# Optimization experiments

Measured on AMD Instinct MI355X. Metric: run time of the kernel, lower is better.

## Reference

```python
import jax, jax.numpy as jnp
import numpy as np
import math

D_MODEL = 128
N_HEADS = 8
HEAD_DIM = D_MODEL // N_HEADS


def setup_inputs() -> dict:
    key = jax.random.key(0)
    ks = jax.random.split(key, 16)
    B, N, D = 8, 1024, D_MODEL
    s = 1.0 / math.sqrt(D)
    inp = {
        "x": jax.random.normal(ks[0], (B, N, D), dtype=jnp.float32),
        "adj_mask": jax.random.randint(ks[1], (B, N, N), 0, 2, dtype=jnp.int32),
        "edge_weights": jax.random.uniform(ks[2], (B, N, N), dtype=jnp.float32),
        "Wq": jax.random.normal(ks[3], (D, D), dtype=jnp.float32) * s,
        "bq": jnp.zeros((D,), jnp.float32),
        "Wk": jax.random.normal(ks[4], (D, D), dtype=jnp.float32) * s,
        "bk": jnp.zeros((D,), jnp.float32),
        "Wv": jax.random.normal(ks[5], (D, D), dtype=jnp.float32) * s,
        "bv": jnp.zeros((D,), jnp.float32),
        "Wo": jax.random.normal(ks[6], (D, D), dtype=jnp.float32) * s,
        "bo": jnp.zeros((D,), jnp.float32),
        "We": jax.random.normal(ks[7], (N_HEADS,), dtype=jnp.float32),  # edge_proj weight (n_heads,1) squeezed
        "be": jnp.zeros((N_HEADS,), jnp.float32),                       # edge_proj bias
    }
    return inp


def reference(x, adj_mask, edge_weights, Wq, bq, Wk, bk, Wv, bv, Wo, bo, We, be):
    B, N, D = x.shape
    H, hd = N_HEADS, HEAD_DIM
    scale = math.sqrt(hd)
    # projections -> (B, H, N, hd)
    Q = (x @ Wq + bq).reshape(B, N, H, hd).transpose(0, 2, 1, 3)
    K = (x @ Wk + bk).reshape(B, N, H, hd).transpose(0, 2, 1, 3)
    V = (x @ Wv + bv).reshape(B, N, H, hd).transpose(0, 2, 1, 3)
    # scores (B, H, N, N)
    scores = jnp.einsum('bhnd,bhmd->bhnm', Q, K) / scale
    # edge bias: Linear(1, H) applied per edge, permuted to (B, H, N, N)
    edge_bias = edge_weights[:, None, :, :] * We[None, :, None, None] + be[None, :, None, None]
    scores = scores + edge_bias
    # adjacency masking
    scores = jnp.where(adj_mask[:, None, :, :] == 0, -jnp.inf, scores)
    attn = jax.nn.softmax(scores, axis=-1)  # dropout=0 (eval)
    out = jnp.einsum('bhnm,bhmd->bhnd', attn, V)
    out = out.transpose(0, 2, 1, 3).reshape(B, N, D)
    return out @ Wo + bo
```

## Files before the change

kernel.cpp:

```cpp
#include <hip/hip_runtime.h>
#include <hip/hip_bf16.h>

typedef __attribute__((ext_vector_type(4))) short bf16x4;
typedef __attribute__((ext_vector_type(4))) float f32x4;
typedef __attribute__((ext_vector_type(4))) int i32x4;

#define LOG2E 1.4426950408889634f
#define SMAX 8.0f

static __device__ inline f32x4 mfma16(bf16x4 a, bf16x4 b, f32x4 c) {
  return __builtin_amdgcn_mfma_f32_16x16x16bf16_1k(a, b, c, 0, 0, 0);
}
static __device__ inline ushort f2bfu(float f) {
  __hip_bfloat16 h = __float2bfloat16(f);
  return *(ushort*)&h;
}
static __device__ __forceinline__ void dma16(const void* g, void* l) {
  __builtin_amdgcn_global_load_lds(
      (const __attribute__((address_space(1))) void*)g,
      (__attribute__((address_space(3))) void*)l, 16, 0, 0);
}

__global__ __launch_bounds__(256) void gemm_qkv(
    const float* __restrict__ x,
    const float* __restrict__ Wq, const float* __restrict__ bq,
    const float* __restrict__ Wk, const float* __restrict__ bk,
    const float* __restrict__ Wv, const float* __restrict__ bv,
    ushort* __restrict__ Qs, ushort* __restrict__ Kt, ushort* __restrict__ Vt) {
  const int which = blockIdx.x >> 10;
  const int bid = blockIdx.x & 1023;
  const int tid = threadIdx.x;
  const int l = tid & 63, w = tid >> 6;
  const int lm = l & 15, g = l >> 4;
  const int tile = bid * 4 + w;
  const int mt = tile >> 3, nt = tile & 7;
  const int row = mt * 16 + lm;
  const int col = nt * 16 + lm;

  const float* W = (which == 0) ? Wq : (which == 1) ? Wk : Wv;
  const float* bias = (which == 0) ? bq : (which == 1) ? bk : bv;

  f32x4 acc = {0.f, 0.f, 0.f, 0.f};
#pragma unroll
  for (int ks = 0; ks < 8; ++ks) {
    f32x4 av = *(const f32x4*)(x + (size_t)row * 128 + ks * 16 + g * 4);
    bf16x4 a;
    a[0] = (short)f2bfu(av[0]); a[1] = (short)f2bfu(av[1]);
    a[2] = (short)f2bfu(av[2]); a[3] = (short)f2bfu(av[3]);
    const float* wp = W + (size_t)(ks * 16 + g * 4) * 128 + col;
    bf16x4 b;
    b[0] = (short)f2bfu(wp[0]);   b[1] = (short)f2bfu(wp[128]);
    b[2] = (short)f2bfu(wp[256]); b[3] = (short)f2bfu(wp[384]);
    acc = mfma16(a, b, acc);
  }
  const float bv_ = bias[col];
  const float alpha = (which == 0) ? 0.25f * LOG2E : 1.0f;
  float v0 = (acc[0] + bv_) * alpha, v1 = (acc[1] + bv_) * alpha;
  float v2 = (acc[2] + bv_) * alpha, v3 = (acc[3] + bv_) * alpha;
  const int mb = mt * 16;

  if (which == 0) {
    Qs[(size_t)(mb + g * 4 + 0) * 128 + col] = f2bfu(v0);
    Qs[(size_t)(mb + g * 4 + 1) * 128 + col] = f2bfu(v1);
    Qs[(size_t)(mb + g * 4 + 2) * 128 + col] = f2bfu(v2);
    Qs[(size_t)(mb + g * 4 + 3) * 128 + col] = f2bfu(v3);
  } else if (which == 1) {
    const size_t kb = ((size_t)((mb >> 10) * 8 + nt) * 1024 + ((mb & 1023) + g * 4));
    Kt[(kb + 0) * 16 + lm] = f2bfu(v0);
    Kt[(kb + 1) * 16 + lm] = f2bfu(v1);
    Kt[(kb + 2) * 16 + lm] = f2bfu(v2);
    Kt[(kb + 3) * 16 + lm] = f2bfu(v3);
  } else {
    const size_t addr = ((size_t)((mb >> 10) * 8 + nt) * 16 + ((mb & 1023) >> 6)) * 1024
                        + (size_t)lm * 64 + (mb & 63) + g * 4;
    bf16x4 vv;
    vv[0] = (short)f2bfu(v0); vv[1] = (short)f2bfu(v1);
    vv[2] = (short)f2bfu(v2); vv[3] = (short)f2bfu(v3);
    *(bf16x4*)(Vt + addr) = vv;
  }
}

#define BUFB 40960

__global__ __launch_bounds__(512) void attn_kernel(
    const ushort* __restrict__ Qs, const ushort* __restrict__ Kt,
    const ushort* __restrict__ Vt, const int* __restrict__ adj,
    const float* __restrict__ edge, const float* __restrict__ We,
    const float* __restrict__ Wo, const float* __restrict__ bo,
    float* __restrict__ out) {
  __shared__ __align__(16) char smem[2 * BUFB];

  const int tid = threadIdx.x;
  const int l = tid & 63, h = tid >> 6;
  const int lm = l & 15, g = l >> 4;
  const int b = blockIdx.x >> 6;
  const int m0 = (blockIdx.x & 63) * 16;

  const float Weh = We[h] * LOG2E;
  const bf16x4 qf = *(const bf16x4*)(Qs + ((size_t)b * 1024 + m0 + lm) * 128 + h * 16 + g * 4);

  const ushort* kt0 = Kt + ((size_t)b * 8 + h) * 16384 + l * 8;
  const int dv = l >> 3, mv = l & 7;
  const int voff = dv * 64 + (((mv * 2) ^ (dv & 6)) * 4);
  const ushort* vt0 = Vt + ((size_t)b * 8 + h) * 16384 + voff;
  const int hh = h & 3;
  const int sr = hh * 4 + (l >> 4);
  const int sci = ((l & 15) * 4) ^ ((sr & 7) << 3);
  const int* ssrc = ((h < 4) ? adj : (const int*)edge)
                    + (size_t)b * 1048576 + (size_t)(m0 + sr) * 1024 + sci;

  char* kdst = smem + h * 2048;
  char* vdst = smem + 16384 + h * 2048;
  char* sdst = smem + ((h < 4) ? 32768 : 36864) + hh * 1024;

  float lsum = 0.f;
  f32x4 oacc = {0.f, 0.f, 0.f, 0.f};
  const f32x4 cinit = {-SMAX, -SMAX, -SMAX, -SMAX};

  auto stage = [&](int T) {
    const int bo_ = (T & 1) * BUFB;
    const ushort* ks = kt0 + (size_t)T * 1024;
    const ushort* vs = vt0 + (size_t)T * 1024;
    dma16(ks,        kdst + bo_);
    dma16(ks + 512,  kdst + bo_ + 1024);
    dma16(vs,        vdst + bo_);
    dma16(vs + 512,  vdst + bo_ + 1024);
    dma16(ssrc + T * 64, sdst + bo_);
  };

  auto compute = [&](int bi) {
    const char* base = smem + bi * BUFB;
    const char* kls = base + h * 2048;
    const char* vls = base + 16384 + h * 2048;
    const int* als = (const int*)(base + 32768);
    const int* els = (const int*)(base + 36864);
    const int xorv = (lm & 7) << 3;

    f32x4 st[4];
    bf16x4 vfr[4];
#pragma unroll
    for (int t = 0; t < 4; ++t) {
      bf16x4 kf = *(const bf16x4*)(kls + (t * 16 + lm) * 32 + g * 8);
      st[t] = mfma16(kf, qf, cinit);
      vfr[t] = *(const bf16x4*)(vls + lm * 128 + (((t * 4 + g) ^ (lm & 6)) * 8));
    }
#pragma unroll
    for (int t = 0; t < 4; ++t) {
      const int ci = (t * 16 + g * 4) ^ xorv;
      const i32x4 a4 = *(const i32x4*)(als + lm * 64 + ci);
      const i32x4 e4i = *(const i32x4*)(els + lm * 64 + ci);
      const f32x4 e4 = *(const f32x4*)&e4i;
      bf16x4 pf4;
#pragma unroll
      for (int j = 0; j < 4; ++j) {
        float p = __builtin_amdgcn_exp2f(fmaf(e4[j], Weh, st[t][j]));
        p = (a4[j] == 0) ? 0.f : p;
        lsum += p;
        pf4[j] = (short)f2bfu(p);
      }
      oacc = mfma16(vfr[t], pf4, oacc);
    }
  };

  stage(0);
  stage(1);

  for (int ct = 0; ct < 15; ++ct) {
    asm volatile("s_waitcnt vmcnt(5)" ::: "memory");
    __builtin_amdgcn_s_barrier();
    __builtin_amdgcn_sched_barrier(0);
    compute(ct & 1);
    __builtin_amdgcn_s_barrier();
    __builtin_amdgcn_sched_barrier(0);
    if (ct < 14) stage(ct + 2);
  }
  asm volatile("s_waitcnt vmcnt(0)" ::: "memory");
  __builtin_amdgcn_s_barrier();
  __builtin_amdgcn_sched_barrier(0);
  compute(1);

  lsum += __shfl_xor(lsum, 16, 64);
  lsum += __shfl_xor(lsum, 32, 64);
  const float inv = 1.0f / lsum;

  __syncthreads();
  ushort* aot = (ushort*)smem;
  {
    bf16x4 ov;
    ov[0] = (short)f2bfu(oacc[0] * inv);
    ov[1] = (short)f2bfu(oacc[1] * inv);
    ov[2] = (short)f2bfu(oacc[2] * inv);
    ov[3] = (short)f2bfu(oacc[3] * inv);
    *(bf16x4*)(aot + lm * 132 + h * 16 + g * 4) = ov;
  }
  __syncthreads();

  f32x4 acc = {0.f, 0.f, 0.f, 0.f};
#pragma unroll
  for (int ks = 0; ks < 8; ++ks) {
    bf16x4 a = *(const bf16x4*)(aot + lm * 132 + ks * 16 + g * 4);
    const float* wp = Wo + (size_t)(ks * 16 + g * 4) * 128 + h * 16 + lm;
    bf16x4 bfr;
    bfr[0] = (short)f2bfu(wp[0]);   bfr[1] = (short)f2bfu(wp[128]);
    bfr[2] = (short)f2bfu(wp[256]); bfr[3] = (short)f2bfu(wp[384]);
    acc = mfma16(a, bfr, acc);
  }
  const float bv = bo[h * 16 + lm];
  float* op = out + ((size_t)b * 1024 + m0 + g * 4) * 128 + h * 16 + lm;
  op[0 * 128] = acc[0] + bv;
  op[1 * 128] = acc[1] + bv;
  op[2 * 128] = acc[2] + bv;
  op[3 * 128] = acc[3] + bv;
}

extern "C" void kernel_launch(void* const* d_in, const int* in_sizes, int n_in,
                              void* d_out, int out_size, void* d_ws, size_t ws_size,
                              hipStream_t stream) {
  const float* x   = (const float*)d_in[0];
  const int*   adj = (const int*)d_in[1];
  const float* ew  = (const float*)d_in[2];
  const float* Wq  = (const float*)d_in[3];
  const float* bq  = (const float*)d_in[4];
  const float* Wk  = (const float*)d_in[5];
  const float* bk  = (const float*)d_in[6];
  const float* Wv  = (const float*)d_in[7];
  const float* bv  = (const float*)d_in[8];
  const float* Wo  = (const float*)d_in[9];
  const float* bo  = (const float*)d_in[10];
  const float* We  = (const float*)d_in[11];

  const size_t MN = (size_t)8 * 1024 * 128;
  ushort* Qs = (ushort*)d_ws;
  ushort* Kt = Qs + MN;
  ushort* Vt = Kt + MN;

  gemm_qkv<<<3072, 256, 0, stream>>>(x, Wq, bq, Wk, bk, Wv, bv, Qs, Kt, Vt);
  attn_kernel<<<512, 512, 0, stream>>>(Qs, Kt, Vt, adj, ew, We, Wo, bo, (float*)d_out);
}
```

Measured before the change: 52.63 us.

## Process 32 query rows per attention block to reuse K/V tiles

Each attention block now handles two 16-row query sub-tiles instead of one, so every K and V tile staged into LDS feeds twice as many MFMAs. The grid is halved to 256 blocks, the LDS buffer grows to hold a doubled adjacency/edge tile, and each warp issues two DMA loads for the mask/edge data. This cuts redundant global K/V traffic, but 256 blocks of 512 threads may leave some of the GPU's compute units idle and raises per-block register and LDS use.

```diff
diff --git a/kernel.cpp b/kernel.cpp
--- a/kernel.cpp
+++ b/kernel.cpp
@@ -80,7 +80,7 @@
   }
 }
 
-#define BUFB 40960
+#define BUFB 49152
 
 __global__ __launch_bounds__(512) void attn_kernel(
     const ushort* __restrict__ Qs, const ushort* __restrict__ Kt,
@@ -93,28 +93,36 @@
   const int tid = threadIdx.x;
   const int l = tid & 63, h = tid >> 6;
   const int lm = l & 15, g = l >> 4;
-  const int b = blockIdx.x >> 6;
-  const int m0 = (blockIdx.x & 63) * 16;
+  const int b = blockIdx.x >> 5;
+  const int m0 = (blockIdx.x & 31) * 32;
 
   const float Weh = We[h] * LOG2E;
-  const bf16x4 qf = *(const bf16x4*)(Qs + ((size_t)b * 1024 + m0 + lm) * 128 + h * 16 + g * 4);
+  bf16x4 qf0 = *(const bf16x4*)(Qs + ((size_t)b * 1024 + m0 + lm) * 128 + h * 16 + g * 4);
+  bf16x4 qf1 = *(const bf16x4*)(Qs + ((size_t)b * 1024 + m0 + 16 + lm) * 128 + h * 16 + g * 4);
 
   const ushort* kt0 = Kt + ((size_t)b * 8 + h) * 16384 + l * 8;
   const int dv = l >> 3, mv = l & 7;
   const int voff = dv * 64 + (((mv * 2) ^ (dv & 6)) * 4);
   const ushort* vt0 = Vt + ((size_t)b * 8 + h) * 16384 + voff;
+
   const int hh = h & 3;
-  const int sr = hh * 4 + (l >> 4);
-  const int sci = ((l & 15) * 4) ^ ((sr & 7) << 3);
-  const int* ssrc = ((h < 4) ? adj : (const int*)edge)
-                    + (size_t)b * 1048576 + (size_t)(m0 + sr) * 1024 + sci;
+  const int d0 = hh * 2, d1 = d0 + 1;
+  const int row0 = 4 * d0 + (l >> 4), row1 = 4 * d1 + (l >> 4);
+  const int gr0 = (l & 15) ^ ((row0 & 7) << 1);
+  const int gr1 = (l & 15) ^ ((row1 & 7) << 1);
+  const int* sbase = ((h < 4) ? adj : (const int*)edge)
+                     + (size_t)b * 1048576 + (size_t)m0 * 1024;
+  const int* ssrc0 = sbase + (size_t)row0 * 1024 + gr0 * 4;
+  const int* ssrc1 = sbase + (size_t)row1 * 1024 + gr1 * 4;
 
   char* kdst = smem + h * 2048;
   char* vdst = smem + 16384 + h * 2048;
-  char* sdst = smem + ((h < 4) ? 32768 : 36864) + hh * 1024;
-
-  float lsum = 0.f;
-  f32x4 oacc = {0.f, 0.f, 0.f, 0.f};
+  char* sreg = smem + ((h < 4) ? 32768 : 40960);
+  char* sdst0 = sreg + d0 * 1024;
+  char* sdst1 = sreg + d1 * 1024;
+
+  float lsum0 = 0.f, lsum1 = 0.f;
+  f32x4 oacc0 = {0.f, 0.f, 0.f, 0.f}, oacc1 = {0.f, 0.f, 0.f, 0.f};
   const f32x4 cinit = {-SMAX, -SMAX, -SMAX, -SMAX};
 
   auto stage = [&](int T) {
@@ -125,7 +133,8 @@
     dma16(ks + 512,  kdst + bo_ + 1024);
     dma16(vs,        vdst + bo_);
     dma16(vs + 512,  vdst + bo_ + 1024);
-    dma16(ssrc + T * 64, sdst + bo_);
+    dma16(ssrc0 + T * 64, sdst0 + bo_);
+    dma16(ssrc1 + T * 64, sdst1 + bo_);
   };
 
   auto compute = [&](int bi) {
@@ -133,32 +142,41 @@
     const char* kls = base + h * 2048;
     const char* vls = base + 16384 + h * 2048;
     const int* als = (const int*)(base + 32768);
-    const int* els = (const int*)(base + 36864);
+    const int* els = (const int*)(base + 40960);
     const int xorv = (lm & 7) << 3;
 
-    f32x4 st[4];
-    bf16x4 vfr[4];
+    bf16x4 kf[4], vfr[4];
 #pragma unroll
     for (int t = 0; t < 4; ++t) {
-      bf16x4 kf = *(const bf16x4*)(kls + (t * 16 + lm) * 32 + g * 8);
-      st[t] = mfma16(kf, qf, cinit);
+      kf[t]  = *(const bf16x4*)(kls + (t * 16 + lm) * 32 + g * 8);
       vfr[t] = *(const bf16x4*)(vls + lm * 128 + (((t * 4 + g) ^ (lm & 6)) * 8));
     }
 #pragma unroll
-    for (int t = 0; t < 4; ++t) {
-      const int ci = (t * 16 + g * 4) ^ xorv;
-      const i32x4 a4 = *(const i32x4*)(als + lm * 64 + ci);
-      const i32x4 e4i = *(const i32x4*)(els + lm * 64 + ci);
-      const f32x4 e4 = *(const f32x4*)&e4i;
-      bf16x4 pf4;
-#pragma unroll
-      for (int j = 0; j < 4; ++j) {
-        float p = __builtin_amdgcn_exp2f(fmaf(e4[j], Weh, st[t][j]));
-        p = (a4[j] == 0) ? 0.f : p;
-        lsum += p;
-        pf4[j] = (short)f2bfu(p);
+    for (int s = 0; s < 2; ++s) {
+      const bf16x4 qf = s ? qf1 : qf0;
+      f32x4 st[4];
+#pragma unroll
+      for (int t = 0; t < 4; ++t) st[t] = mfma16(kf[t], qf, cinit);
+      float lacc = 0.f;
+      f32x4 oac = s ? oacc1 : oacc0;
+#pragma unroll
+      for (int t = 0; t < 4; ++t) {
+        const int ci = (t * 16 + g * 4) ^ xorv;
+        const int ro = (16 * s + lm) * 64;
+        const i32x4 a4 = *(const i32x4*)(als + ro + ci);
+        const i32x4 e4i = *(const i32x4*)(els + ro + ci);
+        const f32x4 e4 = *(const f32x4*)&e4i;
+        bf16x4 pf4;
+#pragma unroll
+        for (int j = 0; j < 4; ++j) {
+          float p = __builtin_amdgcn_exp2f(fmaf(e4[j], Weh, st[t][j]));
+          p = (a4[j] == 0) ? 0.f : p;
+          lacc += p;
+          pf4[j] = (short)f2bfu(p);
+        }
+        oac = mfma16(vfr[t], pf4, oac);
       }
-      oacc = mfma16(vfr[t], pf4, oacc);
+      if (s) { oacc1 = oac; lsum1 += lacc; } else { oacc0 = oac; lsum0 += lacc; }
     }
   };
 
@@ -166,7 +184,7 @@
   stage(1);
 
   for (int ct = 0; ct < 15; ++ct) {
-    asm volatile("s_waitcnt vmcnt(5)" ::: "memory");
+    asm volatile("s_waitcnt vmcnt(6)" ::: "memory");
     __builtin_amdgcn_s_barrier();
     __builtin_amdgcn_sched_barrier(0);
     compute(ct & 1);
@@ -179,38 +197,52 @@
   __builtin_amdgcn_sched_barrier(0);
   compute(1);
 
-  lsum += __shfl_xor(lsum, 16, 64);
-  lsum += __shfl_xor(lsum, 32, 64);
-  const float inv = 1.0f / lsum;
+  lsum0 += __shfl_xor(lsum0, 16, 64);
+  lsum0 += __shfl_xor(lsum0, 32, 64);
+  lsum1 += __shfl_xor(lsum1, 16, 64);
+  lsum1 += __shfl_xor(lsum1, 32, 64);
+  const float inv0 = 1.0f / lsum0, inv1 = 1.0f / lsum1;
 
   __syncthreads();
   ushort* aot = (ushort*)smem;
   {
     bf16x4 ov;
-    ov[0] = (short)f2bfu(oacc[0] * inv);
-    ov[1] = (short)f2bfu(oacc[1] * inv);
-    ov[2] = (short)f2bfu(oacc[2] * inv);
-    ov[3] = (short)f2bfu(oacc[3] * inv);
-    *(bf16x4*)(aot + lm * 132 + h * 16 + g * 4) = ov;
+    ov[0] = (short)f2bfu(oacc0[0] * inv0);
+    ov[1] = (short)f2bfu(oacc0[1] * inv0);
+    ov[2] = (short)f2bfu(oacc0[2] * inv0);
+    ov[3] = (short)f2bfu(oacc0[3] * inv0);
+    *(bf16x4*)(aot + (lm) * 132 + h * 16 + g * 4) = ov;
+    ov[0] = (short)f2bfu(oacc1[0] * inv1);
+    ov[1] = (short)f2bfu(oacc1[1] * inv1);
+    ov[2] = (short)f2bfu(oacc1[2] * inv1);
+    ov[3] = (short)f2bfu(oacc1[3] * inv1);
+    *(bf16x4*)(aot + (16 + lm) * 132 + h * 16 + g * 4) = ov;
   }
   __syncthreads();
 
-  f32x4 acc = {0.f, 0.f, 0.f, 0.f};
+  f32x4 acc0 = {0.f, 0.f, 0.f, 0.f}, acc1 = {0.f, 0.f, 0.f, 0.f};
 #pragma unroll
   for (int ks = 0; ks < 8; ++ks) {
-    bf16x4 a = *(const bf16x4*)(aot + lm * 132 + ks * 16 + g * 4);
     const float* wp = Wo + (size_t)(ks * 16 + g * 4) * 128 + h * 16 + lm;
     bf16x4 bfr;
     bfr[0] = (short)f2bfu(wp[0]);   bfr[1] = (short)f2bfu(wp[128]);
     bfr[2] = (short)f2bfu(wp[256]); bfr[3] = (short)f2bfu(wp[384]);
-    acc = mfma16(a, bfr, acc);
+    bf16x4 a0 = *(const bf16x4*)(aot + lm * 132 + ks * 16 + g * 4);
+    bf16x4 a1 = *(const bf16x4*)(aot + (16 + lm) * 132 + ks * 16 + g * 4);
+    acc0 = mfma16(a0, bfr, acc0);
+    acc1 = mfma16(a1, bfr, acc1);
   }
   const float bv = bo[h * 16 + lm];
-  float* op = out + ((size_t)b * 1024 + m0 + g * 4) * 128 + h * 16 + lm;
-  op[0 * 128] = acc[0] + bv;
-  op[1 * 128] = acc[1] + bv;
-  op[2 * 128] = acc[2] + bv;
-  op[3 * 128] = acc[3] + bv;
+  float* op0 = out + ((size_t)b * 1024 + m0 + g * 4) * 128 + h * 16 + lm;
+  float* op1 = op0 + 16 * 128;
+  op0[0 * 128] = acc0[0] + bv;
+  op0[1 * 128] = acc0[1] + bv;
+  op0[2 * 128] = acc0[2] + bv;
+  op0[3 * 128] = acc0[3] + bv;
+  op1[0 * 128] = acc1[0] + bv;
+  op1[1 * 128] = acc1[1] + bv;
+  op1[2 * 128] = acc1[2] + bv;
+  op1[3 * 128] = acc1[3] + bv;
 }
 
 extern "C" void kernel_launch(void* const* d_in, const int* in_sizes, int n_in,
@@ -235,5 +267,5 @@
   ushort* Vt = Kt + MN;
 
   gemm_qkv<<<3072, 256, 0, stream>>>(x, Wq, bq, Wk, bk, Wv, bv, Qs, Kt, Vt);
-  attn_kernel<<<512, 512, 0, stream>>>(Qs, Kt, Vt, adj, ew, We, Wo, bo, (float*)d_out);
-}
+  attn_kernel<<<256, 512, 0, stream>>>(Qs, Kt, Vt, adj, ew, We, Wo, bo, (float*)d_out);
+}
```

New measurement: 52.44 us. No clear change (-0.4%).

## Load K/V fragments directly from global and triple-buffer only mask/edge tiles

Applied to the files above, without the earlier changes.

K and V fragments are now read straight from global memory into registers per tile, no longer DMA'd into LDS. Only the adjacency and edge tiles still go through LDS, now in a three-slot ring, so each iteration needs one barrier instead of two. The loop is fully unrolled with hand-tuned vmcnt waits that account for the extra in-flight register loads. This shrinks LDS use and removes the LDS round trip for K/V. In exchange, exposed global-load latency can stall the MFMAs, and the hardcoded vmcnt counts are fragile.

```diff
diff --git a/kernel.cpp b/kernel.cpp
--- a/kernel.cpp
+++ b/kernel.cpp
@@ -80,7 +80,7 @@
   }
 }
 
-#define BUFB 40960
+#define SB 8192
 
 __global__ __launch_bounds__(512) void attn_kernel(
     const ushort* __restrict__ Qs, const ushort* __restrict__ Kt,
@@ -88,7 +88,7 @@
     const float* __restrict__ edge, const float* __restrict__ We,
     const float* __restrict__ Wo, const float* __restrict__ bo,
     float* __restrict__ out) {
-  __shared__ __align__(16) char smem[2 * BUFB];
+  __shared__ __align__(16) char smem[3 * SB];
 
   const int tid = threadIdx.x;
   const int l = tid & 63, h = tid >> 6;
@@ -98,51 +98,52 @@
 
   const float Weh = We[h] * LOG2E;
   const bf16x4 qf = *(const bf16x4*)(Qs + ((size_t)b * 1024 + m0 + lm) * 128 + h * 16 + g * 4);
-
-  const ushort* kt0 = Kt + ((size_t)b * 8 + h) * 16384 + l * 8;
-  const int dv = l >> 3, mv = l & 7;
-  const int voff = dv * 64 + (((mv * 2) ^ (dv & 6)) * 4);
-  const ushort* vt0 = Vt + ((size_t)b * 8 + h) * 16384 + voff;
+  __builtin_amdgcn_sched_barrier(0);
+
+  const ushort* kp = Kt + ((size_t)b * 8 + h) * 16384 + lm * 16 + g * 4;
+  const ushort* vp = Vt + ((size_t)b * 8 + h) * 16384 + lm * 64 + g * 4;
+
   const int hh = h & 3;
   const int sr = hh * 4 + (l >> 4);
   const int sci = ((l & 15) * 4) ^ ((sr & 7) << 3);
   const int* ssrc = ((h < 4) ? adj : (const int*)edge)
                     + (size_t)b * 1048576 + (size_t)(m0 + sr) * 1024 + sci;
-
-  char* kdst = smem + h * 2048;
-  char* vdst = smem + 16384 + h * 2048;
-  char* sdst = smem + ((h < 4) ? 32768 : 36864) + hh * 1024;
+  const int sdoff = ((h < 4) ? 0 : 4096) + hh * 1024;
 
   float lsum = 0.f;
   f32x4 oacc = {0.f, 0.f, 0.f, 0.f};
   const f32x4 cinit = {-SMAX, -SMAX, -SMAX, -SMAX};
 
   auto stage = [&](int T) {
-    const int bo_ = (T & 1) * BUFB;
-    const ushort* ks = kt0 + (size_t)T * 1024;
-    const ushort* vs = vt0 + (size_t)T * 1024;
-    dma16(ks,        kdst + bo_);
-    dma16(ks + 512,  kdst + bo_ + 1024);
-    dma16(vs,        vdst + bo_);
-    dma16(vs + 512,  vdst + bo_ + 1024);
-    dma16(ssrc + T * 64, sdst + bo_);
+    dma16(ssrc + T * 64, smem + (T % 3) * SB + sdoff);
   };
 
-  auto compute = [&](int bi) {
-    const char* base = smem + bi * BUFB;
-    const char* kls = base + h * 2048;
-    const char* vls = base + 16384 + h * 2048;
-    const int* als = (const int*)(base + 32768);
-    const int* els = (const int*)(base + 36864);
+  stage(0);
+  stage(1);
+
+#pragma unroll
+  for (int ct = 0; ct < 16; ++ct) {
+    if (ct == 0)       asm volatile("s_waitcnt vmcnt(1)" ::: "memory");
+    else if (ct == 1)  asm volatile("s_waitcnt vmcnt(9)" ::: "memory");
+    else if (ct == 15) asm volatile("s_waitcnt vmcnt(16)" ::: "memory");
+    else               asm volatile("s_waitcnt vmcnt(17)" ::: "memory");
+    __builtin_amdgcn_s_barrier();
+    __builtin_amdgcn_sched_barrier(0);
+
+    if (ct < 14) stage(ct + 2);
+    __builtin_amdgcn_sched_barrier(0);
+
+    const int* als = (const int*)(smem + (ct % 3) * SB);
+    const int* els = (const int*)(smem + (ct % 3) * SB + 4096);
     const int xorv = (lm & 7) << 3;
 
     f32x4 st[4];
     bf16x4 vfr[4];
 #pragma unroll
     for (int t = 0; t < 4; ++t) {
-      bf16x4 kf = *(const bf16x4*)(kls + (t * 16 + lm) * 32 + g * 8);
+      bf16x4 kf = *(const bf16x4*)(kp + ct * 1024 + t * 256);
+      vfr[t] = *(const bf16x4*)(vp + ct * 1024 + t * 16);
       st[t] = mfma16(kf, qf, cinit);
-      vfr[t] = *(const bf16x4*)(vls + lm * 128 + (((t * 4 + g) ^ (lm & 6)) * 8));
     }
 #pragma unroll
     for (int t = 0; t < 4; ++t) {
@@ -160,24 +161,7 @@
       }
       oacc = mfma16(vfr[t], pf4, oacc);
     }
-  };
-
-  stage(0);
-  stage(1);
-
-  for (int ct = 0; ct < 15; ++ct) {
-    asm volatile("s_waitcnt vmcnt(5)" ::: "memory");
-    __builtin_amdgcn_s_barrier();
-    __builtin_amdgcn_sched_barrier(0);
-    compute(ct & 1);
-    __builtin_amdgcn_s_barrier();
-    __builtin_amdgcn_sched_barrier(0);
-    if (ct < 14) stage(ct + 2);
-  }
-  asm volatile("s_waitcnt vmcnt(0)" ::: "memory");
-  __builtin_amdgcn_s_barrier();
-  __builtin_amdgcn_sched_barrier(0);
-  compute(1);
+  }
 
   lsum += __shfl_xor(lsum, 16, 64);
   lsum += __shfl_xor(lsum, 32, 64);
```

Result: slower. 100.3 us (+90.5%).
